# Kernel tuning notes

Measured on AMD Instinct MI355X. Metric: run time of the kernel, lower is better.

Reference implementation:

```python
import jax, jax.numpy as jnp
import numpy as np

B, S, H, E, K = 4, 2048, 1024, 8, 2


def setup_inputs() -> dict:
    key = jax.random.key(0)
    k0, k1, k2 = jax.random.split(key, 3)
    x = jax.random.normal(k0, (B, S, H), dtype=jnp.float32)
    # gate: Linear(H -> E); torch stores W as [out,in], we keep [E,H]
    gate_w = jax.random.normal(k1, (E, H), dtype=jnp.float32) * 0.02
    gate_b = jnp.zeros((E,), dtype=jnp.float32)
    # experts: E x Linear(H -> H); stored as [E, H_in, H_out]
    expert_w = jax.random.normal(k2, (E, H, H), dtype=jnp.float32) * 0.02
    expert_b = jnp.zeros((E, H), dtype=jnp.float32)
    return {"x": x, "gate_w": gate_w, "gate_b": gate_b,
            "expert_w": expert_w, "expert_b": expert_b}


def reference(x, gate_w, gate_b, expert_w, expert_b):
    bsz, seq_len, h = x.shape
    xt = x.reshape(-1, h)                      # [T, H]
    T = xt.shape[0]

    # router (moe_router): softmax -> top-k -> renormalize
    logits = xt @ gate_w.T + gate_b            # [T, E]
    routing_probs = jax.nn.softmax(logits, axis=-1)
    top_k_probs, top_k_index = jax.lax.top_k(routing_probs, K)
    top_k_probs = top_k_probs / jnp.sum(top_k_probs, axis=1, keepdims=True)
    top_k_probs = top_k_probs.astype(x.dtype)

    # combine weights: scatter normalized top-k probs into [T, E]
    rows = jnp.arange(T)[:, None]
    combine = jnp.zeros((T, E), dtype=x.dtype).at[rows, top_k_index].add(top_k_probs)

    # per-expert FFN over all tokens, then weighted combine
    # (equivalent math to the gather / index_add loop: zero weights contribute zero)
    y = jnp.einsum('th,eho->teo', xt, expert_w) + expert_b[None, :, :]  # [T, E, H]
    out = jnp.einsum('te,teh->th', combine, y)                          # [T, H]

    final_output = out.reshape(bsz, seq_len, h)
    return final_output, top_k_index, routing_probs
```

## Files before the change

kernel.cpp:

```cpp
#include <hip/hip_runtime.h>
#include <hip/hip_bf16.h>
#include <stdint.h>

typedef unsigned short ushort_t;
typedef __bf16 bf16x8 __attribute__((ext_vector_type(8)));
typedef float f32x4 __attribute__((ext_vector_type(4)));

#define T_TOK 8192
#define H_DIM 1024
#define E_EXP 8
#define BM 128
#define BN 128
#define BK 64
#define NKT (H_DIM / BK)
#define NWG_G 2304

#define CNT_STRIDE 64
#define RTOK 32
#define RBLOCKS (T_TOK / RTOK)
#define TP_BLOCKS ((H_DIM / 32) * (H_DIM / 32) * E_EXP)

static __device__ __forceinline__ ushort_t f2bf(float f) {
  union { float f; uint32_t u; } c; c.f = f;
  uint32_t u = c.u;
  uint32_t r = u + 0x7FFFu + ((u >> 16) & 1u);
  return (ushort_t)(r >> 16);
}

__global__ __launch_bounds__(256) void router_transpose(
    const float* __restrict__ x, const float* __restrict__ gw,
    const float* __restrict__ gb, const float* __restrict__ ew,
    float* __restrict__ out_idx, float* __restrict__ out_probs,
    int* __restrict__ counts, int* __restrict__ tok, float* __restrict__ wts,
    ushort_t* __restrict__ xg, ushort_t* __restrict__ wT)
{
  __shared__ ushort_t xrow[RTOK][H_DIM];
  __shared__ int   sm_eid[RTOK * 2];
  __shared__ float sm_wt[RTOK * 2];
  __shared__ int   sm_dst[RTOK * 2];
  __shared__ int   lcnt[E_EXP], lbase[E_EXP], lpos[E_EXP];
  __shared__ float tile[32][33];

  const int tid = threadIdx.x;

  if (blockIdx.x >= RBLOCKS) {
    const int tb = blockIdx.x - RBLOCKS;
    const int e = tb >> 10;
    const int n0 = (tb & 31) * 32, k0 = ((tb >> 5) & 31) * 32;
    const float* we = ew + (size_t)e * H_DIM * H_DIM;
    ushort_t* wTe = wT + (size_t)e * H_DIM * H_DIM;
    const int tx = tid & 31, ty = tid >> 5;
#pragma unroll
    for (int i = 0; i < 4; i++)
      tile[ty + 8 * i][tx] = we[(size_t)(k0 + ty + 8 * i) * H_DIM + n0 + tx];
    __syncthreads();
#pragma unroll
    for (int i = 0; i < 4; i++)
      wTe[(size_t)(n0 + ty + 8 * i) * H_DIM + k0 + tx] = f2bf(tile[tx][ty + 8 * i]);
    return;
  }

  const int wave = tid >> 6, l = tid & 63;
  if (tid < E_EXP) { lcnt[tid] = 0; lpos[tid] = 0; }
  __syncthreads();

  const int t0 = blockIdx.x * RTOK;
  for (int it = 0; it < RTOK / 4; it++) {
    const int lt = wave * (RTOK / 4) + it;
    const int t = t0 + lt;
    const float* xt = x + (size_t)t * H_DIM;
    float acc[E_EXP];
#pragma unroll
    for (int e = 0; e < E_EXP; e++) acc[e] = 0.f;
#pragma unroll
    for (int i = 0; i < 4; i++) {
      const int h = (i * 64 + l) * 4;
      const float4 xv = *reinterpret_cast<const float4*>(xt + h);
      ushort4 b;
      b.x = f2bf(xv.x); b.y = f2bf(xv.y); b.z = f2bf(xv.z); b.w = f2bf(xv.w);
      *reinterpret_cast<ushort4*>(&xrow[lt][h]) = b;
#pragma unroll
      for (int e = 0; e < E_EXP; e++) {
        const float4 g = *reinterpret_cast<const float4*>(gw + e * H_DIM + h);
        acc[e] += xv.x * g.x + xv.y * g.y + xv.z * g.z + xv.w * g.w;
      }
    }
#pragma unroll
    for (int e = 0; e < E_EXP; e++) {
      float v = acc[e];
#pragma unroll
      for (int off = 32; off; off >>= 1) v += __shfl_xor(v, off);
      acc[e] = v;
    }
    if (l == 0) {
      float lg[E_EXP], pb[E_EXP];
      float m = -1e30f;
#pragma unroll
      for (int e = 0; e < E_EXP; e++) { lg[e] = acc[e] + gb[e]; m = fmaxf(m, lg[e]); }
      float s = 0.f;
#pragma unroll
      for (int e = 0; e < E_EXP; e++) { pb[e] = expf(lg[e] - m); s += pb[e]; }
      const float inv = 1.f / s;
#pragma unroll
      for (int e = 0; e < E_EXP; e++) {
        pb[e] *= inv;
        out_probs[(size_t)t * E_EXP + e] = pb[e];
      }
      int i0 = 0; float p0 = pb[0];
#pragma unroll
      for (int e = 1; e < E_EXP; e++) if (pb[e] > p0) { p0 = pb[e]; i0 = e; }
      int i1 = -1; float p1 = -1.f;
#pragma unroll
      for (int e = 0; e < E_EXP; e++) if (e != i0 && pb[e] > p1) { p1 = pb[e]; i1 = e; }
      out_idx[(size_t)t * 2 + 0] = (float)i0;
      out_idx[(size_t)t * 2 + 1] = (float)i1;
      const float rn = 1.f / (p0 + p1);
      sm_eid[lt * 2 + 0] = i0; sm_wt[lt * 2 + 0] = p0 * rn;
      sm_eid[lt * 2 + 1] = i1; sm_wt[lt * 2 + 1] = p1 * rn;
    }
  }
  __syncthreads();

  if (tid < RTOK * 2) atomicAdd(&lcnt[sm_eid[tid]], 1);
  __syncthreads();
  if (tid < E_EXP) lbase[tid] = atomicAdd(&counts[tid * CNT_STRIDE], lcnt[tid]);
  __syncthreads();
  if (tid < RTOK * 2) {
    const int e = sm_eid[tid];
    const int p = lbase[e] + atomicAdd(&lpos[e], 1);
    const int dst = e * T_TOK + p;
    tok[dst] = (t0 + (tid >> 1)) * 2 + (tid & 1);
    wts[dst] = sm_wt[tid];
    sm_dst[tid] = dst;
  }
  __syncthreads();

  for (int ent0 = 0; ent0 < RTOK * 2; ent0 += 4) {
    const int ent = ent0 + wave;
    const int dst = sm_dst[ent];
    const ushort_t* src = &xrow[ent >> 1][0];
    ushort_t* d = xg + (size_t)dst * H_DIM;
    const int o = l * 16;
    *reinterpret_cast<int4*>(d + o) = *reinterpret_cast<const int4*>(src + o);
    *reinterpret_cast<int4*>(d + o + 8) =
        *reinterpret_cast<const int4*>(src + o + 8);
  }
}

#define GLDS16(gp, lp)                                                         \
  __builtin_amdgcn_global_load_lds(                                            \
      (const __attribute__((address_space(1))) void*)(gp),                     \
      (__attribute__((address_space(3))) void*)(lp), 16, 0, 0)

__global__ __launch_bounds__(256, 3) void moe_gemm(
    const ushort_t* __restrict__ xg, const ushort_t* __restrict__ wT,
    const float* __restrict__ bias, int* __restrict__ counts,
    const int* __restrict__ tok, const float* __restrict__ wts,
    ushort_t* __restrict__ y)
{
  __shared__ __align__(16) ushort_t As[2 * 4096];
  __shared__ __align__(16) ushort_t Bs[2 * 4096];
  __shared__ int stok[BM];
  __shared__ float swt[BM];
  __shared__ int s_spill;

  const int tid = threadIdx.x;
  const int bid = blockIdx.x;

  int ne[E_EXP], fl[E_EXP];
#pragma unroll
  for (int i = 0; i < E_EXP; i++) {
    ne[i] = counts[i * CNT_STRIDE];
    fl[i] = ne[i] >> 7;
  }

  const int l = tid & 63;
  const int wid = tid >> 6;
  const int fr = l & 15;
  const int g = l >> 4;

  if (bid < 2048) {
    int e = bid & 7;
    int q = bid >> 3;
    const int home = fl[e] * 8;
    if (q >= (home < 256 ? home : 256)) {
      int sc[E_EXP], spill_total = 0;
#pragma unroll
      for (int i = 0; i < E_EXP; i++) {
        sc[i] = fl[i] * 8 > 256 ? fl[i] * 8 - 256 : 0;
        spill_total += sc[i];
      }
      if (spill_total == 0) return;
      if (tid == 0) s_spill = atomicAdd(&counts[520], 1);
      __syncthreads();
      int k = s_spill;
      if (k >= spill_total) return;
      int done = 0;
#pragma unroll
      for (int i = 0; i < E_EXP; i++) {
        if (!done) { if (k < sc[i]) { e = i; done = 1; } else k -= sc[i]; }
      }
      q = 256 + k;
    }
    const int mt = q >> 3;
    const int nt = q & 7;

    if (tid < BM) {
      stok[tid] = tok[e * T_TOK + mt * BM + tid];
      swt[tid] = wts[e * T_TOK + mt * BM + tid];
    }
    __syncthreads();

    const int r0 = tid >> 2;
    const int cp = (tid & 3) ^ ((tid >> 3) & 3);
    const ushort_t* wTe = wT + (size_t)e * H_DIM * H_DIM;
    const ushort_t* aBase = xg + (size_t)(e * T_TOK + mt * BM) * H_DIM;
    const ushort_t* aP0 = aBase + (size_t)r0 * H_DIM + cp * 8;
    const ushort_t* aP1 = aBase + (size_t)(r0 + 64) * H_DIM + cp * 8;
    const ushort_t* bP0 = wTe + (size_t)(nt * BN + r0) * H_DIM + cp * 8;
    const ushort_t* bP1 = wTe + (size_t)(nt * BN + r0 + 64) * H_DIM + cp * 8;
    const int d0 = tid * 8;
    const int d1 = (tid + 256) * 8;

#define STAGE8(t)                                                              \
  do {                                                                         \
    GLDS16(aP0 + (t) * BK +  0, &As[0 * 4096 + d0]);                           \
    GLDS16(aP1 + (t) * BK +  0, &As[0 * 4096 + d1]);                           \
    GLDS16(aP0 + (t) * BK + 32, &As[1 * 4096 + d0]);                           \
    GLDS16(aP1 + (t) * BK + 32, &As[1 * 4096 + d1]);                           \
    GLDS16(bP0 + (t) * BK +  0, &Bs[0 * 4096 + d0]);                           \
    GLDS16(bP1 + (t) * BK +  0, &Bs[0 * 4096 + d1]);                           \
    GLDS16(bP0 + (t) * BK + 32, &Bs[1 * 4096 + d0]);                           \
    GLDS16(bP1 + (t) * BK + 32, &Bs[1 * 4096 + d1]);                           \
  } while (0)

    const int wm = wid >> 1, wn = wid & 1;
    const int sl = g ^ ((l >> 1) & 3);
    const int arow0 = wm * 64 + fr;
    const int brow0 = wn * 64 + fr;

    f32x4 acc[4][4] = {};

#pragma unroll 1
    for (int t = 0; t < NKT; ++t) {
      if (t) __syncthreads();
      STAGE8(t);
      __syncthreads();
#pragma unroll
      for (int kk = 0; kk < 2; kk++) {
        bf16x8 af[4], bv[4];
#pragma unroll
        for (int mi = 0; mi < 4; mi++)
          af[mi] = *reinterpret_cast<const bf16x8*>(
              &As[kk * 4096 + (arow0 + mi * 16) * 32 + sl * 8]);
#pragma unroll
        for (int nj = 0; nj < 4; nj++)
          bv[nj] = *reinterpret_cast<const bf16x8*>(
              &Bs[kk * 4096 + (brow0 + nj * 16) * 32 + sl * 8]);
        __builtin_amdgcn_s_setprio(1);
#pragma unroll
        for (int mi = 0; mi < 4; mi++)
#pragma unroll
          for (int nj = 0; nj < 4; nj++)
            acc[mi][nj] = __builtin_amdgcn_mfma_f32_16x16x32_bf16(
                af[mi], bv[nj], acc[mi][nj], 0, 0, 0);
        __builtin_amdgcn_s_setprio(0);
      }
    }

    float bias4[4];
#pragma unroll
    for (int nj = 0; nj < 4; nj++)
      bias4[nj] = bias[e * H_DIM + nt * BN + wn * 64 + nj * 16 + fr];
#pragma unroll
    for (int mi = 0; mi < 4; mi++) {
      const int rr0 = wm * 64 + mi * 16 + g * 4;
#pragma unroll
      for (int r = 0; r < 4; r++) {
        const int row = rr0 + r;
        const float wgt = swt[row];
        ushort_t* yr = y + (size_t)stok[row] * H_DIM;
#pragma unroll
        for (int nj = 0; nj < 4; nj++) {
          const int n = nt * BN + wn * 64 + nj * 16 + fr;
          yr[n] = f2bf(wgt * (acc[mi][nj][r] + bias4[nj]));
        }
      }
    }
  } else {
    const int e = bid & 7;
    const int tq = (bid - 2048) >> 3;
    const int rem = ne[e] - (fl[e] << 7);
    const int tcnt = (rem + 63) >> 6;
    if (tq >= tcnt * 8) return;
    const int mtt = tq >> 3;
    const int ntt = tq & 7;
    const int row0 = (fl[e] << 7) + mtt * 64;
    int valid = ne[e] - row0; if (valid > 64) valid = 64;

    if (tid < 64) {
      int slot = row0 + tid;
      if (slot >= ne[e]) slot = ne[e] - 1;
      stok[tid] = tok[e * T_TOK + slot];
      swt[tid] = wts[e * T_TOK + slot];
    }
    __syncthreads();

    const ushort_t* wTe = wT + (size_t)e * H_DIM * H_DIM;
    const int trow = tid >> 3;
    const int tlc = (tid & 7) ^ (trow & 7);
    int tsl0 = row0 + trow;       if (tsl0 >= ne[e]) tsl0 = ne[e] - 1;
    int tsl1 = row0 + trow + 32;  if (tsl1 >= ne[e]) tsl1 = ne[e] - 1;
    const ushort_t* taS0 = xg + (size_t)(e * T_TOK + tsl0) * H_DIM + tlc * 8;
    const ushort_t* taS1 = xg + (size_t)(e * T_TOK + tsl1) * H_DIM + tlc * 8;
    const ushort_t* tbS0 = wTe + (size_t)(ntt * 128 + trow) * H_DIM + tlc * 8;
    const ushort_t* tbS1 = tbS0 + (size_t)32 * H_DIM;
    const ushort_t* tbS2 = tbS0 + (size_t)64 * H_DIM;
    const ushort_t* tbS3 = tbS0 + (size_t)96 * H_DIM;

#define TSTAGE1(t)                                                             \
  do {                                                                         \
    GLDS16(taS0 + (t) * BK, &As[tid * 8]);                                     \
    GLDS16(taS1 + (t) * BK, &As[(tid + 256) * 8]);                             \
    GLDS16(tbS0 + (t) * BK, &Bs[tid * 8]);                                     \
    GLDS16(tbS1 + (t) * BK, &Bs[(tid + 256) * 8]);                             \
    GLDS16(tbS2 + (t) * BK, &Bs[(tid + 512) * 8]);                             \
    GLDS16(tbS3 + (t) * BK, &Bs[(tid + 768) * 8]);                             \
  } while (0)

    const int tph0 = (g ^ (fr & 7)) * 8;
    const int tph1 = ((4 ^ g) ^ (fr & 7)) * 8;

    f32x4 tacc[2][4] = {};

#pragma unroll 1
    for (int t = 0; t < NKT; ++t) {
      if (t) __syncthreads();
      TSTAGE1(t);
      __syncthreads();
#pragma unroll
      for (int kk = 0; kk < 2; kk++) {
        const int ph = kk ? tph1 : tph0;
#pragma unroll
        for (int nf = 0; nf < 2; nf++) {
          const bf16x8 tbv = *reinterpret_cast<const bf16x8*>(
              &Bs[(wid * 32 + nf * 16 + fr) * 64 + ph]);
#pragma unroll
          for (int mi = 0; mi < 4; mi++) {
            const bf16x8 tav = *reinterpret_cast<const bf16x8*>(
                &As[(mi * 16 + fr) * 64 + ph]);
            tacc[nf][mi] = __builtin_amdgcn_mfma_f32_16x16x32_bf16(
                tav, tbv, tacc[nf][mi], 0, 0, 0);
          }
        }
      }
    }

#pragma unroll
    for (int nf = 0; nf < 2; nf++) {
      const int ncol = ntt * 128 + wid * 32 + nf * 16 + fr;
      const float bs = bias[e * H_DIM + ncol];
#pragma unroll
      for (int mi = 0; mi < 4; mi++) {
        const int rb = mi * 16 + g * 4;
#pragma unroll
        for (int r = 0; r < 4; r++) {
          const int row = rb + r;
          if (row < valid) {
            ushort_t* yr = y + (size_t)stok[row] * H_DIM;
            yr[ncol] = f2bf(swt[row] * (tacc[nf][mi][r] + bs));
          }
        }
      }
    }
  }
}

__global__ __launch_bounds__(256) void combine_kernel(
    const ushort_t* __restrict__ y, float* __restrict__ out)
{
  const int t = blockIdx.x;
  const ushort_t* r0 = y + (size_t)(t * 2) * H_DIM;
  const ushort_t* r1 = r0 + H_DIM;
  float* o = out + (size_t)t * H_DIM;
  const int h = threadIdx.x * 4;
  const ushort4 u0 = *reinterpret_cast<const ushort4*>(r0 + h);
  const ushort4 u1 = *reinterpret_cast<const ushort4*>(r1 + h);
  float4 v;
  union { uint32_t u; float f; } c;
  c.u = (uint32_t)u0.x << 16; v.x = c.f; c.u = (uint32_t)u1.x << 16; v.x += c.f;
  c.u = (uint32_t)u0.y << 16; v.y = c.f; c.u = (uint32_t)u1.y << 16; v.y += c.f;
  c.u = (uint32_t)u0.z << 16; v.z = c.f; c.u = (uint32_t)u1.z << 16; v.z += c.f;
  c.u = (uint32_t)u0.w << 16; v.w = c.f; c.u = (uint32_t)u1.w << 16; v.w += c.f;
  *reinterpret_cast<float4*>(o + h) = v;
}

extern "C" void kernel_launch(void* const* d_in, const int* in_sizes, int n_in,
                              void* d_out, int out_size, void* d_ws, size_t ws_size,
                              hipStream_t stream)
{
  const float* x  = (const float*)d_in[0];
  const float* gw = (const float*)d_in[1];
  const float* gb = (const float*)d_in[2];
  const float* ew = (const float*)d_in[3];
  const float* eb = (const float*)d_in[4];

  float* out = (float*)d_out;
  float* out_final = out;
  float* out_idx   = out + (size_t)T_TOK * H_DIM;
  float* out_probs = out_idx + (size_t)T_TOK * 2;

  char* ws = (char*)d_ws;
  size_t off = 0;
  int*      counts  = (int*)(ws + off); off += 4096;
  int*      tok     = (int*)(ws + off); off += (size_t)E_EXP * T_TOK * 4;
  float*    wts     = (float*)(ws + off); off += (size_t)E_EXP * T_TOK * 4;
  ushort_t* wT      = (ushort_t*)(ws + off); off += (size_t)E_EXP * H_DIM * H_DIM * 2;
  ushort_t* y       = (ushort_t*)(ws + off); off += (size_t)T_TOK * 2 * H_DIM * 2;
  ushort_t* xg      = (ushort_t*)(ws + off); off += (size_t)E_EXP * T_TOK * H_DIM * 2;

  hipMemsetAsync(counts, 0, 4096, stream);

  router_transpose<<<RBLOCKS + TP_BLOCKS, 256, 0, stream>>>(
      x, gw, gb, ew, out_idx, out_probs, counts, tok, wts, xg, wT);
  moe_gemm<<<NWG_G, 256, 0, stream>>>(xg, wT, eb, counts, tok, wts, y);
  combine_kernel<<<T_TOK, 256, 0, stream>>>(y, out_final);
}
```

Before: 96.17 us.

## Gather A rows by token index in GEMM instead of materializing permuted copy

```diff
diff --git a/kernel.cpp b/kernel.cpp
--- a/kernel.cpp
+++ b/kernel.cpp
@@ -32,12 +32,10 @@
     const float* __restrict__ gb, const float* __restrict__ ew,
     float* __restrict__ out_idx, float* __restrict__ out_probs,
     int* __restrict__ counts, int* __restrict__ tok, float* __restrict__ wts,
-    ushort_t* __restrict__ xg, ushort_t* __restrict__ wT)
+    ushort_t* __restrict__ x_bf, ushort_t* __restrict__ wT)
 {
-  __shared__ ushort_t xrow[RTOK][H_DIM];
   __shared__ int   sm_eid[RTOK * 2];
   __shared__ float sm_wt[RTOK * 2];
-  __shared__ int   sm_dst[RTOK * 2];
   __shared__ int   lcnt[E_EXP], lbase[E_EXP], lpos[E_EXP];
   __shared__ float tile[32][33];
 
@@ -78,7 +76,7 @@
       const float4 xv = *reinterpret_cast<const float4*>(xt + h);
       ushort4 b;
       b.x = f2bf(xv.x); b.y = f2bf(xv.y); b.z = f2bf(xv.z); b.w = f2bf(xv.w);
-      *reinterpret_cast<ushort4*>(&xrow[lt][h]) = b;
+      *reinterpret_cast<ushort4*>(x_bf + (size_t)t * H_DIM + h) = b;
 #pragma unroll
       for (int e = 0; e < E_EXP; e++) {
         const float4 g = *reinterpret_cast<const float4*>(gw + e * H_DIM + h);
@@ -131,19 +129,6 @@
     const int dst = e * T_TOK + p;
     tok[dst] = (t0 + (tid >> 1)) * 2 + (tid & 1);
     wts[dst] = sm_wt[tid];
-    sm_dst[tid] = dst;
-  }
-  __syncthreads();
-
-  for (int ent0 = 0; ent0 < RTOK * 2; ent0 += 4) {
-    const int ent = ent0 + wave;
-    const int dst = sm_dst[ent];
-    const ushort_t* src = &xrow[ent >> 1][0];
-    ushort_t* d = xg + (size_t)dst * H_DIM;
-    const int o = l * 16;
-    *reinterpret_cast<int4*>(d + o) = *reinterpret_cast<const int4*>(src + o);
-    *reinterpret_cast<int4*>(d + o + 8) =
-        *reinterpret_cast<const int4*>(src + o + 8);
   }
 }
 
@@ -152,8 +137,8 @@
       (const __attribute__((address_space(1))) void*)(gp),                     \
       (__attribute__((address_space(3))) void*)(lp), 16, 0, 0)
 
-__global__ __launch_bounds__(256, 3) void moe_gemm(
-    const ushort_t* __restrict__ xg, const ushort_t* __restrict__ wT,
+__global__ __launch_bounds__(256, 4) void moe_gemm(
+    const ushort_t* __restrict__ x_bf, const ushort_t* __restrict__ wT,
     const float* __restrict__ bias, int* __restrict__ counts,
     const int* __restrict__ tok, const float* __restrict__ wts,
     ushort_t* __restrict__ y)
@@ -214,9 +199,8 @@
     const int r0 = tid >> 2;
     const int cp = (tid & 3) ^ ((tid >> 3) & 3);
     const ushort_t* wTe = wT + (size_t)e * H_DIM * H_DIM;
-    const ushort_t* aBase = xg + (size_t)(e * T_TOK + mt * BM) * H_DIM;
-    const ushort_t* aP0 = aBase + (size_t)r0 * H_DIM + cp * 8;
-    const ushort_t* aP1 = aBase + (size_t)(r0 + 64) * H_DIM + cp * 8;
+    const ushort_t* aP0 = x_bf + (size_t)(stok[r0] >> 1) * H_DIM + cp * 8;
+    const ushort_t* aP1 = x_bf + (size_t)(stok[r0 + 64] >> 1) * H_DIM + cp * 8;
     const ushort_t* bP0 = wTe + (size_t)(nt * BN + r0) * H_DIM + cp * 8;
     const ushort_t* bP1 = wTe + (size_t)(nt * BN + r0 + 64) * H_DIM + cp * 8;
     const int d0 = tid * 8;
@@ -309,10 +293,8 @@
     const ushort_t* wTe = wT + (size_t)e * H_DIM * H_DIM;
     const int trow = tid >> 3;
     const int tlc = (tid & 7) ^ (trow & 7);
-    int tsl0 = row0 + trow;       if (tsl0 >= ne[e]) tsl0 = ne[e] - 1;
-    int tsl1 = row0 + trow + 32;  if (tsl1 >= ne[e]) tsl1 = ne[e] - 1;
-    const ushort_t* taS0 = xg + (size_t)(e * T_TOK + tsl0) * H_DIM + tlc * 8;
-    const ushort_t* taS1 = xg + (size_t)(e * T_TOK + tsl1) * H_DIM + tlc * 8;
+    const ushort_t* taS0 = x_bf + (size_t)(stok[trow] >> 1) * H_DIM + tlc * 8;
+    const ushort_t* taS1 = x_bf + (size_t)(stok[trow + 32] >> 1) * H_DIM + tlc * 8;
     const ushort_t* tbS0 = wTe + (size_t)(ntt * 128 + trow) * H_DIM + tlc * 8;
     const ushort_t* tbS1 = tbS0 + (size_t)32 * H_DIM;
     const ushort_t* tbS2 = tbS0 + (size_t)64 * H_DIM;
@@ -415,14 +397,14 @@
   int*      counts  = (int*)(ws + off); off += 4096;
   int*      tok     = (int*)(ws + off); off += (size_t)E_EXP * T_TOK * 4;
   float*    wts     = (float*)(ws + off); off += (size_t)E_EXP * T_TOK * 4;
+  ushort_t* x_bf    = (ushort_t*)(ws + off); off += (size_t)T_TOK * H_DIM * 2;
   ushort_t* wT      = (ushort_t*)(ws + off); off += (size_t)E_EXP * H_DIM * H_DIM * 2;
   ushort_t* y       = (ushort_t*)(ws + off); off += (size_t)T_TOK * 2 * H_DIM * 2;
-  ushort_t* xg      = (ushort_t*)(ws + off); off += (size_t)E_EXP * T_TOK * H_DIM * 2;
 
   hipMemsetAsync(counts, 0, 4096, stream);
 
   router_transpose<<<RBLOCKS + TP_BLOCKS, 256, 0, stream>>>(
-      x, gw, gb, ew, out_idx, out_probs, counts, tok, wts, xg, wT);
-  moe_gemm<<<NWG_G, 256, 0, stream>>>(xg, wT, eb, counts, tok, wts, y);
+      x, gw, gb, ew, out_idx, out_probs, counts, tok, wts, x_bf, wT);
+  moe_gemm<<<NWG_G, 256, 0, stream>>>(x_bf, wT, eb, counts, tok, wts, y);
   combine_kernel<<<T_TOK, 256, 0, stream>>>(y, out_final);
 }
```

New measurement: 93.84 us. 2.4% less time.
